# Kernel optimization log

Hardware: AMD Instinct MI355X
Metric: run time of the kernel (lower is better)

Reference implementation:

```python
import jax, jax.numpy as jnp
import numpy as np

C = 64
C8 = C // 8
N, H, W = 4, 512, 512


def conv1x1(x, w, b):
    # x: [N,C,H,W], w: [O,C], b: [O]
    return jnp.einsum('nchw,oc->nohw', x, w) + b[None, :, None, None]


def time_attention(x, qw, qb, kw, kb, vw, vb, gamma):
    # attention over the H axis; feature dim is (C//8)*W
    q = conv1x1(x, qw, qb)                     # [N,C8,H,W]
    k = conv1x1(x, kw, kb)                     # [N,C8,H,W]
    v = conv1x1(x, vw, vb)                     # [N,C,H,W]
    energy = jnp.einsum('nchw,ncgw->nhg', q, k)   # [N,H,H]
    attn = jax.nn.softmax(energy, axis=-1)
    out = jnp.einsum('ncgw,nhg->nchw', v, attn)   # [N,C,H,W]
    return gamma * out + x


def freq_attention(x, qw, qb, kw, kb, vw, vb, gamma):
    # attention over the W axis; feature dim is (C//8)*H
    q = conv1x1(x, qw, qb)
    k = conv1x1(x, kw, kb)
    v = conv1x1(x, vw, vb)
    energy = jnp.einsum('nchw,nchv->nwv', q, k)   # [N,W,W]
    attn = jax.nn.softmax(energy, axis=-1)
    out = jnp.einsum('nchv,nwv->nchw', v, attn)
    return gamma * out + x


def setup_inputs() -> dict:
    key = jax.random.key(0)
    ks = jax.random.split(key, 8)
    s = 0.05
    return {
        'x': jax.random.normal(ks[0], (N, C, H, W), dtype=jnp.float32),
        'tq_w': jax.random.normal(ks[1], (C8, C), dtype=jnp.float32) * s,
        'tq_b': jnp.zeros((C8,), jnp.float32),
        'tk_w': jax.random.normal(ks[2], (C8, C), dtype=jnp.float32) * s,
        'tk_b': jnp.zeros((C8,), jnp.float32),
        'tv_w': jax.random.normal(ks[3], (C, C), dtype=jnp.float32) * s,
        'tv_b': jnp.zeros((C,), jnp.float32),
        't_gamma': jnp.ones((1,), jnp.float32) * 0.5,
        'fq_w': jax.random.normal(ks[4], (C8, C), dtype=jnp.float32) * s,
        'fq_b': jnp.zeros((C8,), jnp.float32),
        'fk_w': jax.random.normal(ks[5], (C8, C), dtype=jnp.float32) * s,
        'fk_b': jnp.zeros((C8,), jnp.float32),
        'fv_w': jax.random.normal(ks[6], (C, C), dtype=jnp.float32) * s,
        'fv_b': jnp.zeros((C,), jnp.float32),
        'f_gamma': jnp.ones((1,), jnp.float32) * 0.5,
    }


def reference(x, tq_w, tq_b, tk_w, tk_b, tv_w, tv_b, t_gamma,
              fq_w, fq_b, fk_w, fk_b, fv_w, fv_b, f_gamma):
    t = time_attention(x, tq_w, tq_b, tk_w, tk_b, tv_w, tv_b, t_gamma)
    f = freq_attention(x, fq_w, fq_b, fk_w, fk_b, fv_w, fv_b, f_gamma)
    return x + t + f
```

## Files before the change

kernel.cpp:

```cpp
#include <hip/hip_runtime.h>
#include <stdint.h>

#define HW 262144
#define LDIM 512

typedef __bf16 bf16x8 __attribute__((ext_vector_type(8)));
typedef float f32x4 __attribute__((ext_vector_type(4)));
typedef short s16x8 __attribute__((ext_vector_type(8)));
typedef short s16x4 __attribute__((ext_vector_type(4)));

__device__ __forceinline__ unsigned short f2bf(float f) {
  union { float f; unsigned u; } v; v.f = f;
  unsigned r = v.u + 0x7fffu + ((v.u >> 16) & 1u);
  return (unsigned short)(r >> 16);
}

__device__ __forceinline__ float bf2f(short s) {
  union { unsigned u; float f; } v;
  v.u = ((unsigned)(unsigned short)s) << 16;
  return v.f;
}

__device__ __forceinline__ s16x8 pack_bf8(float4 a, float4 b) {
  s16x8 r;
  r[0] = (short)f2bf(a.x); r[1] = (short)f2bf(a.y);
  r[2] = (short)f2bf(a.z); r[3] = (short)f2bf(a.w);
  r[4] = (short)f2bf(b.x); r[5] = (short)f2bf(b.y);
  r[6] = (short)f2bf(b.z); r[7] = (short)f2bf(b.w);
  return r;
}

__device__ __forceinline__ f32x4 mfma16(bf16x8 a, bf16x8 b, f32x4 c) {
  return __builtin_amdgcn_mfma_f32_16x16x32_bf16(a, b, c, 0, 0, 0);
}

__device__ __forceinline__ void gl_lds16(const short* g, short* l) {
  __builtin_amdgcn_global_load_lds(
      (const __attribute__((address_space(1))) void*)g,
      (__attribute__((address_space(3))) void*)l, 16, 0, 0);
}

__global__ __launch_bounds__(256) void cast_k(const float* __restrict__ x,
                                              short* __restrict__ xb,
                                              short* __restrict__ xt) {
  __shared__ short L[64][72];
  int z = blockIdx.z;
  int h0 = blockIdx.y * 64, w0 = blockIdx.x * 64;
  int tid = threadIdx.x;
  size_t base = (size_t)z * HW;
  int hl = tid >> 4;
  int wl = (tid & 15) * 4;
#pragma unroll
  for (int it = 0; it < 4; ++it) {
    int h = h0 + hl + it * 16;
    float4 v = *(const float4*)(x + base + (size_t)h * 512 + w0 + wl);
    s16x4 b;
    b[0] = (short)f2bf(v.x); b[1] = (short)f2bf(v.y);
    b[2] = (short)f2bf(v.z); b[3] = (short)f2bf(v.w);
    *(s16x4*)(xb + base + (size_t)h * 512 + w0 + wl) = b;
    L[wl + 0][hl + it * 16] = b[0];
    L[wl + 1][hl + it * 16] = b[1];
    L[wl + 2][hl + it * 16] = b[2];
    L[wl + 3][hl + it * 16] = b[3];
  }
  __syncthreads();
#pragma unroll
  for (int it = 0; it < 4; ++it) {
    int w = hl + it * 16;
    s16x4 v = *(const s16x4*)(&L[w][wl]);
    *(s16x4*)(xt + base + (size_t)(w0 + w) * 512 + h0 + wl) = v;
  }
}

__global__ __launch_bounds__(256) void prep_k(const float* __restrict__ tvw,
                                              const float* __restrict__ fvw,
                                              short* __restrict__ Wvb) {
  int t = threadIdx.x;
#pragma unroll
  for (int i = 0; i < 2; ++i) {
    int idx = (i * 256 + t) * 8;
    float4 a = *(const float4*)(tvw + idx);
    float4 b = *(const float4*)(tvw + idx + 4);
    *(s16x8*)(Wvb + idx) = pack_bf8(a, b);
    a = *(const float4*)(fvw + idx);
    b = *(const float4*)(fvw + idx + 4);
    *(s16x8*)(Wvb + 4096 + idx) = pack_bf8(a, b);
  }
}

template<bool OBF>
__global__ __launch_bounds__(256, 4) void gemm_a(
    const short* __restrict__ A0, long az, int zshA,
    const short* __restrict__ B0, long bz, int zshB,
    void* __restrict__ C0, long cz) {
  __shared__ __align__(16) short As[128 * 32];
  __shared__ __align__(16) short Bs[128 * 32];
  int tid = threadIdx.x;
  int z = blockIdx.z;
  int m0g = blockIdx.y * 128, n0g = blockIdx.x * 128;
  const short* Abz = A0 + (size_t)(z >> zshA) * (size_t)az;
  const short* Bbz = B0 + (size_t)(z >> zshB) * (size_t)bz;
  int lane = tid & 63, wv = tid >> 6;
  int wm = (wv >> 1) * 64, wn = (wv & 1) * 64;
  int fr = lane & 15, q = lane >> 4;

  int srow = lane >> 2;
  int sch = (lane & 3) * 8;
  const short* ga0 = Abz + (size_t)(m0g + wv * 32 + srow) * 512 + sch;
  const short* ga1 = ga0 + 16 * 512;
  const short* gb0 = Bbz + (size_t)(n0g + wv * 32 + srow) * 512 + sch;
  const short* gb1 = gb0 + 16 * 512;
  short* la0 = As + (wv * 32) * 32;
  short* la1 = As + (wv * 32 + 16) * 32;
  short* lb0 = Bs + (wv * 32) * 32;
  short* lb1 = Bs + (wv * 32 + 16) * 32;

  f32x4 acc[4][4];
#pragma unroll
  for (int mi = 0; mi < 4; ++mi)
#pragma unroll
    for (int ni = 0; ni < 4; ++ni) acc[mi][ni] = (f32x4){0.f, 0.f, 0.f, 0.f};

  for (int kk = 0; kk < 512; kk += 32) {
    gl_lds16(ga0 + kk, la0);
    gl_lds16(ga1 + kk, la1);
    gl_lds16(gb0 + kk, lb0);
    gl_lds16(gb1 + kk, lb1);
    __syncthreads();
    bf16x8 af[4], bg[4];
#pragma unroll
    for (int mi = 0; mi < 4; ++mi)
      af[mi] = *(const bf16x8*)(As + (wm + mi * 16 + fr) * 32 + q * 8);
#pragma unroll
    for (int ni = 0; ni < 4; ++ni)
      bg[ni] = *(const bf16x8*)(Bs + (wn + ni * 16 + fr) * 32 + q * 8);
#pragma unroll
    for (int mi = 0; mi < 4; ++mi)
#pragma unroll
      for (int ni = 0; ni < 4; ++ni)
        acc[mi][ni] = mfma16(af[mi], bg[ni], acc[mi][ni]);
    __syncthreads();
  }

  size_t coff = (size_t)z * (size_t)cz;
#pragma unroll
  for (int mi = 0; mi < 4; ++mi)
#pragma unroll
    for (int ni = 0; ni < 4; ++ni) {
      int row = m0g + wm + mi * 16 + q * 4;
      int col = n0g + wn + ni * 16 + fr;
#pragma unroll
      for (int r = 0; r < 4; ++r) {
        float v = acc[mi][ni][r];
        if constexpr (OBF) {
          ((short*)C0)[coff + (size_t)(row + r) * LDIM + col] = (short)f2bf(v);
        } else {
          ((float*)C0)[coff + (size_t)(row + r) * LDIM + col] = v;
        }
      }
    }
}

__global__ __launch_bounds__(256, 2) void gemm_t(
    const short* __restrict__ A0, long az,
    const short* __restrict__ B0, long bz,
    float* __restrict__ C0, long cz) {
  __shared__ __align__(16) short As[128 * 40];
  __shared__ __align__(16) short Bs[128 * 40];
  int tid = threadIdx.x;
  int z = blockIdx.z;
  int m0g = blockIdx.y * 128, n0g = blockIdx.x * 128;
  const short* Abz = A0 + (size_t)z * (size_t)az;
  const short* Bbz = B0 + (size_t)z * (size_t)bz;
  int lane = tid & 63, wv = tid >> 6;
  int wm = (wv >> 1) * 64, wn = (wv & 1) * 64;
  int fr = lane & 15, q = lane >> 4;
  int mp = (tid & 63) * 2, k0 = (tid >> 6) * 8;

  f32x4 acc[4][4];
#pragma unroll
  for (int mi = 0; mi < 4; ++mi)
#pragma unroll
    for (int ni = 0; ni < 4; ++ni) acc[mi][ni] = (f32x4){0.f, 0.f, 0.f, 0.f};

  for (int kk = 0; kk < 512; kk += 32) {
    {
      const short* s = Abz + (size_t)(kk + k0) * 512 + m0g + mp;
      s16x8 c0, c1;
#pragma unroll
      for (int j = 0; j < 8; ++j) {
        unsigned v = *(const unsigned*)(s + (size_t)j * 512);
        c0[j] = (short)(v & 0xffffu);
        c1[j] = (short)(v >> 16);
      }
      *(s16x8*)(As + mp * 40 + k0) = c0;
      *(s16x8*)(As + (mp + 1) * 40 + k0) = c1;
    }
    {
      const short* s = Bbz + (size_t)(kk + k0) * 512 + n0g + mp;
      s16x8 c0, c1;
#pragma unroll
      for (int j = 0; j < 8; ++j) {
        unsigned v = *(const unsigned*)(s + (size_t)j * 512);
        c0[j] = (short)(v & 0xffffu);
        c1[j] = (short)(v >> 16);
      }
      *(s16x8*)(Bs + mp * 40 + k0) = c0;
      *(s16x8*)(Bs + (mp + 1) * 40 + k0) = c1;
    }
    __syncthreads();
    bf16x8 af[4], bg[4];
#pragma unroll
    for (int mi = 0; mi < 4; ++mi)
      af[mi] = *(const bf16x8*)(As + (wm + mi * 16 + fr) * 40 + q * 8);
#pragma unroll
    for (int ni = 0; ni < 4; ++ni)
      bg[ni] = *(const bf16x8*)(Bs + (wn + ni * 16 + fr) * 40 + q * 8);
#pragma unroll
    for (int mi = 0; mi < 4; ++mi)
#pragma unroll
      for (int ni = 0; ni < 4; ++ni)
        acc[mi][ni] = mfma16(af[mi], bg[ni], acc[mi][ni]);
    __syncthreads();
  }

  size_t coff = (size_t)z * (size_t)cz;
#pragma unroll
  for (int mi = 0; mi < 4; ++mi)
#pragma unroll
    for (int ni = 0; ni < 4; ++ni) {
      int row = m0g + wm + mi * 16 + q * 4;
      int col = n0g + wn + ni * 16 + fr;
#pragma unroll
      for (int r = 0; r < 4; ++r)
        C0[coff + (size_t)(row + r) * LDIM + col] = acc[mi][ni][r];
    }
}

__global__ __launch_bounds__(256, 2) void conv_qk_k(
    const short* __restrict__ xb,
    const float* __restrict__ tqw, const float* __restrict__ tqb,
    const float* __restrict__ tkw, const float* __restrict__ tkb,
    const float* __restrict__ fqw, const float* __restrict__ fqb,
    const float* __restrict__ fkw, const float* __restrict__ fkb,
    short* __restrict__ QT, short* __restrict__ KT,
    short* __restrict__ QF, short* __restrict__ KF) {
  __shared__ __align__(16) short As[128 * 72];
  __shared__ __align__(16) short Ws[32 * 72];
  __shared__ float bia[32];
  int tid = threadIdx.x;
  int n = blockIdx.x >> 11;
  int p0 = (blockIdx.x & 2047) << 7;
  {
    int co = tid >> 3, k0 = (tid & 7) * 8;
    const float* wsrc = (co < 8) ? tqw : (co < 16) ? tkw : (co < 24) ? fqw : fkw;
    const float* sp = wsrc + (co & 7) * 64 + k0;
    float4 f0 = *(const float4*)sp;
    float4 f1 = *(const float4*)(sp + 4);
    *(s16x8*)(Ws + co * 72 + k0) = pack_bf8(f0, f1);
    if (tid < 32) {
      const float* bsrc = (tid < 8) ? tqb : (tid < 16) ? tkb : (tid < 24) ? fqb : fkb;
      bia[tid] = bsrc[tid & 7];
    }
  }
  {
    int mp = (tid & 31) * 4, k0 = (tid >> 5) * 8;
    const short* sp = xb + ((size_t)(n * 64 + k0)) * HW + p0 + mp;
    s16x8 t0, t1, t2, t3;
#pragma unroll
    for (int j = 0; j < 8; ++j) {
      s16x4 vv = *(const s16x4*)(sp + (size_t)j * HW);
      t0[j] = vv[0]; t1[j] = vv[1]; t2[j] = vv[2]; t3[j] = vv[3];
    }
    *(s16x8*)(As + (mp + 0) * 72 + k0) = t0;
    *(s16x8*)(As + (mp + 1) * 72 + k0) = t1;
    *(s16x8*)(As + (mp + 2) * 72 + k0) = t2;
    *(s16x8*)(As + (mp + 3) * 72 + k0) = t3;
  }
  __syncthreads();
  int lane = tid & 63, wv = tid >> 6, fr = lane & 15, q = lane >> 4;
  int wm = wv * 32;
  f32x4 acc[2][2];
#pragma unroll
  for (int mi = 0; mi < 2; ++mi)
#pragma unroll
    for (int ni = 0; ni < 2; ++ni) acc[mi][ni] = (f32x4){0.f, 0.f, 0.f, 0.f};
#pragma unroll
  for (int ks = 0; ks < 2; ++ks) {
    bf16x8 af[2], bf_[2];
#pragma unroll
    for (int mi = 0; mi < 2; ++mi)
      af[mi] = *(const bf16x8*)(As + (wm + mi * 16 + fr) * 72 + ks * 32 + q * 8);
#pragma unroll
    for (int ni = 0; ni < 2; ++ni)
      bf_[ni] = *(const bf16x8*)(Ws + (ni * 16 + fr) * 72 + ks * 32 + q * 8);
#pragma unroll
    for (int mi = 0; mi < 2; ++mi)
#pragma unroll
      for (int ni = 0; ni < 2; ++ni)
        acc[mi][ni] = mfma16(af[mi], bf_[ni], acc[mi][ni]);
  }
#pragma unroll
  for (int mi = 0; mi < 2; ++mi)
#pragma unroll
    for (int ni = 0; ni < 2; ++ni) {
      int pl = wm + mi * 16 + q * 4;
      int co = ni * 16 + fr;
      float b = bia[co];
      short* dstt = (co < 8) ? QT : (co < 16) ? KT : (co < 24) ? QF : KF;
      short* d = dstt + ((size_t)(n * 8 + (co & 7))) * HW + p0 + pl;
      s16x4 sv;
#pragma unroll
      for (int r = 0; r < 4; ++r) sv[r] = (short)f2bf(acc[mi][ni][r] + b);
      *(s16x4*)d = sv;
    }
}

__global__ __launch_bounds__(256, 4) void softmax8_k(const float* __restrict__ Ep,
                                                     short* __restrict__ A) {
  int tid = threadIdx.x;
  int lane = tid & 63, wv = tid >> 6;
  int row = blockIdx.x * 4 + wv;
  int n = row >> 9, h = row & 511;
  const float* base = Ep + (size_t)(n * 8) * HW + (size_t)h * 512 + lane * 8;
  float v[8] = {0.f, 0.f, 0.f, 0.f, 0.f, 0.f, 0.f, 0.f};
#pragma unroll
  for (int cc = 0; cc < 8; ++cc) {
    const float* e = base + (size_t)cc * HW;
    float4 a = *(const float4*)e;
    float4 b = *(const float4*)(e + 4);
    v[0] += a.x; v[1] += a.y; v[2] += a.z; v[3] += a.w;
    v[4] += b.x; v[5] += b.y; v[6] += b.z; v[7] += b.w;
  }
  float m = v[0];
#pragma unroll
  for (int j = 1; j < 8; ++j) m = fmaxf(m, v[j]);
#pragma unroll
  for (int off = 32; off >= 1; off >>= 1) m = fmaxf(m, __shfl_xor(m, off));
  float s = 0.f;
#pragma unroll
  for (int j = 0; j < 8; ++j) {
    v[j] = __expf(v[j] - m);
    s += v[j];
  }
#pragma unroll
  for (int off = 32; off >= 1; off >>= 1) s += __shfl_xor(s, off);
  float inv = 1.f / s;
  s16x8 o;
#pragma unroll
  for (int j = 0; j < 8; ++j) o[j] = (short)f2bf(v[j] * inv);
  *(s16x8*)(A + (size_t)row * LDIM + lane * 8) = o;
}

__global__ __launch_bounds__(256, 3) void final_k(
    const short* __restrict__ ZT, const short* __restrict__ ZF,
    const short* __restrict__ xb, const short* __restrict__ Wvb,
    const float* __restrict__ tvb, const float* __restrict__ fvb,
    const float* __restrict__ tg, const float* __restrict__ fg,
    float* __restrict__ outn) {
  __shared__ __align__(16) short Zts[128 * 72];
  __shared__ __align__(16) short Zfs[128 * 72];
  __shared__ float bia[128];
  int tid = threadIdx.x;
  int n = blockIdx.x >> 11;
  int p0 = (blockIdx.x & 2047) << 7;
  if (tid < 128) bia[tid] = (tid < 64) ? tvb[tid] : fvb[tid - 64];
  {
    int mp = (tid & 31) * 4, k0 = (tid >> 5) * 8;
    const short* spT = ZT + ((size_t)(n * 64 + k0)) * HW + p0 + mp;
    const short* spF = ZF + ((size_t)(n * 64 + k0)) * HW + p0 + mp;
    s16x8 t0, t1, t2, t3;
#pragma unroll
    for (int j = 0; j < 8; ++j) {
      s16x4 vv = *(const s16x4*)(spT + (size_t)j * HW);
      t0[j] = vv[0]; t1[j] = vv[1]; t2[j] = vv[2]; t3[j] = vv[3];
    }
    *(s16x8*)(Zts + (mp + 0) * 72 + k0) = t0;
    *(s16x8*)(Zts + (mp + 1) * 72 + k0) = t1;
    *(s16x8*)(Zts + (mp + 2) * 72 + k0) = t2;
    *(s16x8*)(Zts + (mp + 3) * 72 + k0) = t3;
#pragma unroll
    for (int j = 0; j < 8; ++j) {
      s16x4 vv = *(const s16x4*)(spF + (size_t)j * HW);
      t0[j] = vv[0]; t1[j] = vv[1]; t2[j] = vv[2]; t3[j] = vv[3];
    }
    *(s16x8*)(Zfs + (mp + 0) * 72 + k0) = t0;
    *(s16x8*)(Zfs + (mp + 1) * 72 + k0) = t1;
    *(s16x8*)(Zfs + (mp + 2) * 72 + k0) = t2;
    *(s16x8*)(Zfs + (mp + 3) * 72 + k0) = t3;
  }
  __syncthreads();
  int lane = tid & 63, wv = tid >> 6, fr = lane & 15, q = lane >> 4;
  int wm = wv * 32;
  f32x4 at_[2][4], af_[2][4];
#pragma unroll
  for (int mi = 0; mi < 2; ++mi)
#pragma unroll
    for (int ni = 0; ni < 4; ++ni) {
      at_[mi][ni] = (f32x4){0.f, 0.f, 0.f, 0.f};
      af_[mi][ni] = (f32x4){0.f, 0.f, 0.f, 0.f};
    }
#pragma unroll
  for (int ks = 0; ks < 2; ++ks) {
    bf16x8 zt_[2], zf_[2], wt_[4], wf_[4];
#pragma unroll
    for (int mi = 0; mi < 2; ++mi) {
      zt_[mi] = *(const bf16x8*)(Zts + (wm + mi * 16 + fr) * 72 + ks * 32 + q * 8);
      zf_[mi] = *(const bf16x8*)(Zfs + (wm + mi * 16 + fr) * 72 + ks * 32 + q * 8);
    }
#pragma unroll
    for (int ni = 0; ni < 4; ++ni) {
      wt_[ni] = *(const bf16x8*)(Wvb + (ni * 16 + fr) * 64 + ks * 32 + q * 8);
      wf_[ni] = *(const bf16x8*)(Wvb + 4096 + (ni * 16 + fr) * 64 + ks * 32 + q * 8);
    }
#pragma unroll
    for (int mi = 0; mi < 2; ++mi)
#pragma unroll
      for (int ni = 0; ni < 4; ++ni) {
        at_[mi][ni] = mfma16(zt_[mi], wt_[ni], at_[mi][ni]);
        af_[mi][ni] = mfma16(zf_[mi], wf_[ni], af_[mi][ni]);
      }
  }
  float gtv = tg[0], gfv = fg[0];
#pragma unroll
  for (int mi = 0; mi < 2; ++mi)
#pragma unroll
    for (int ni = 0; ni < 4; ++ni) {
      int pl = wm + mi * 16 + q * 4;
      int co = ni * 16 + fr;
      size_t idx = ((size_t)(n * 64 + co)) * HW + p0 + pl;
      s16x4 xv = *(const s16x4*)(xb + idx);
      float bt = bia[co], bff = bia[64 + co];
      float4 ov;
      ov.x = 3.f * bf2f(xv[0]) + gtv * (at_[mi][ni][0] + bt) + gfv * (af_[mi][ni][0] + bff);
      ov.y = 3.f * bf2f(xv[1]) + gtv * (at_[mi][ni][1] + bt) + gfv * (af_[mi][ni][1] + bff);
      ov.z = 3.f * bf2f(xv[2]) + gtv * (at_[mi][ni][2] + bt) + gfv * (af_[mi][ni][2] + bff);
      ov.w = 3.f * bf2f(xv[3]) + gtv * (at_[mi][ni][3] + bt) + gfv * (af_[mi][ni][3] + bff);
      *(float4*)(outn + idx) = ov;
    }
}

extern "C" void kernel_launch(void* const* d_in, const int* in_sizes, int n_in,
                              void* d_out, int out_size, void* d_ws, size_t ws_size,
                              hipStream_t stream) {
  (void)in_sizes; (void)n_in; (void)out_size;
  const float* x   = (const float*)d_in[0];
  const float* tqw = (const float*)d_in[1];
  const float* tqb = (const float*)d_in[2];
  const float* tkw = (const float*)d_in[3];
  const float* tkb = (const float*)d_in[4];
  const float* tvw = (const float*)d_in[5];
  const float* tvb = (const float*)d_in[6];
  const float* tg  = (const float*)d_in[7];
  const float* fqw = (const float*)d_in[8];
  const float* fqb = (const float*)d_in[9];
  const float* fkw = (const float*)d_in[10];
  const float* fkb = (const float*)d_in[11];
  const float* fvw = (const float*)d_in[12];
  const float* fvb = (const float*)d_in[13];
  const float* fg  = (const float*)d_in[14];
  float* out = (float*)d_out;

  const size_t per_n = ((size_t)64 * HW * 2) * 3
                     + ((size_t)8 * HW * 2) * 4
                     + (size_t)HW * 2;
  int nb = (ws_size >= 4 * per_n + 16384) ? 4
         : (ws_size >= 2 * per_n + 16384) ? 2 : 1;

  char* w = (char*)d_ws;
  short* Wvb = (short*)w;
  char* wb = w + 16384;
  size_t sz_x  = (size_t)nb * 64 * HW * 2;
  size_t sz_qk = (size_t)nb * 8 * HW * 2;
  short* xb = (short*)(wb);
  short* ZF = (short*)(wb + sz_x);
  short* xt = ZF;
  short* QT = (short*)(wb + 2 * sz_x);
  short* KT = (short*)(wb + 2 * sz_x + sz_qk);
  short* QF = (short*)(wb + 2 * sz_x + 2 * sz_qk);
  short* KF = (short*)(wb + 2 * sz_x + 3 * sz_qk);
  short* ZT = (short*)(wb + 2 * sz_x + 4 * sz_qk);
  short* Ab = (short*)(wb + 3 * sz_x + 4 * sz_qk);
  float* EbT = (float*)ZT;
  float* EbF = (float*)ZF;

  prep_k<<<dim3(1), dim3(256), 0, stream>>>(tvw, fvw, Wvb);

  for (int n0 = 0; n0 < 4; n0 += nb) {
    const float* xn = x + (size_t)n0 * 64 * HW;
    float* outn = out + (size_t)n0 * 64 * HW;
    cast_k<<<dim3(8, 8, nb * 64), dim3(256), 0, stream>>>(xn, xb, xt);
    conv_qk_k<<<dim3(nb * 2048), dim3(256), 0, stream>>>(
        xb, tqw, tqb, tkw, tkb, fqw, fqb, fkw, fkb, QT, KT, QF, KF);
    gemm_a<false><<<dim3(4, 4, nb * 8), dim3(256), 0, stream>>>(
        QT, (long)HW, 0, KT, (long)HW, 0, EbT, (long)HW);
    softmax8_k<<<dim3(nb * 128), dim3(256), 0, stream>>>(EbT, Ab);
    gemm_a<true><<<dim3(4, 4, nb * 64), dim3(256), 0, stream>>>(
        Ab, (long)HW, 6, xt, (long)HW, 0, ZT, (long)HW);
    gemm_t<<<dim3(4, 4, nb * 8), dim3(256), 0, stream>>>(
        QF, (long)HW, KF, (long)HW, EbF, (long)HW);
    softmax8_k<<<dim3(nb * 128), dim3(256), 0, stream>>>(EbF, Ab);
    gemm_a<true><<<dim3(4, 4, nb * 64), dim3(256), 0, stream>>>(
        xb, (long)HW, 0, Ab, (long)HW, 6, ZF, (long)HW);
    final_k<<<dim3(nb * 2048), dim3(256), 0, stream>>>(
        ZT, ZF, xb, Wvb, tvb, fvb, tg, fg, outn);
  }
}
```

Baseline: 977.1 us.

## Apply value projections before attention and fuse both attention GEMMs with output epilogue

Reorders the computation so the 1x1 value convolutions run before the attention products: frequency V is computed alongside Q/K in one conv kernel, and time V is computed in place on the transposed input. The two attention GEMMs then accumulate into one register tile in a single fused kernel that also adds the residual and biases and writes the fp32 output, which removes the separate final projection kernel and the ZT/ZF intermediates. Gamma is folded into the softmax normalisation, and the energy scratch buffers are placed in the output tensor. The cost is an extra V-conv pass over the input, a loop that stages four tiles per k-step and so uses more LDS, and scalar strided epilogue stores in place of vectorised ones.

```diff
diff --git a/kernel.cpp b/kernel.cpp
--- a/kernel.cpp
+++ b/kernel.cpp
@@ -72,20 +72,163 @@
   }
 }
 
-__global__ __launch_bounds__(256) void prep_k(const float* __restrict__ tvw,
-                                              const float* __restrict__ fvw,
-                                              short* __restrict__ Wvb) {
-  int t = threadIdx.x;
+__global__ __launch_bounds__(256, 2) void conv_qkvf_k(
+    const short* __restrict__ xb,
+    const float* __restrict__ tqw, const float* __restrict__ tqb,
+    const float* __restrict__ tkw, const float* __restrict__ tkb,
+    const float* __restrict__ fqw, const float* __restrict__ fqb,
+    const float* __restrict__ fkw, const float* __restrict__ fkb,
+    const float* __restrict__ fvw,
+    short* __restrict__ QT, short* __restrict__ KT,
+    short* __restrict__ QF, short* __restrict__ KF,
+    short* __restrict__ Vf) {
+  __shared__ __align__(16) short As[128 * 72];
+  __shared__ __align__(16) short Ws[96 * 72];
+  __shared__ float bia[32];
+  int tid = threadIdx.x;
+  int n = blockIdx.x >> 11;
+  int p0 = (blockIdx.x & 2047) << 7;
+#pragma unroll
+  for (int i = 0; i < 3; ++i) {
+    int idx = i * 256 + tid;
+    int co = idx >> 3, k0 = (idx & 7) * 8;
+    const float* wrow = (co < 8)  ? tqw + co * 64
+                      : (co < 16) ? tkw + (co - 8) * 64
+                      : (co < 24) ? fqw + (co - 16) * 64
+                      : (co < 32) ? fkw + (co - 24) * 64
+                                  : fvw + (co - 32) * 64;
+    float4 f0 = *(const float4*)(wrow + k0);
+    float4 f1 = *(const float4*)(wrow + k0 + 4);
+    *(s16x8*)(Ws + co * 72 + k0) = pack_bf8(f0, f1);
+  }
+  if (tid < 32) {
+    const float* bsrc = (tid < 8) ? tqb : (tid < 16) ? tkb : (tid < 24) ? fqb : fkb;
+    bia[tid] = bsrc[tid & 7];
+  }
+  {
+    int mp = (tid & 31) * 4, k0 = (tid >> 5) * 8;
+    const short* sp = xb + ((size_t)(n * 64 + k0)) * HW + p0 + mp;
+    s16x8 t0, t1, t2, t3;
+#pragma unroll
+    for (int j = 0; j < 8; ++j) {
+      s16x4 vv = *(const s16x4*)(sp + (size_t)j * HW);
+      t0[j] = vv[0]; t1[j] = vv[1]; t2[j] = vv[2]; t3[j] = vv[3];
+    }
+    *(s16x8*)(As + (mp + 0) * 72 + k0) = t0;
+    *(s16x8*)(As + (mp + 1) * 72 + k0) = t1;
+    *(s16x8*)(As + (mp + 2) * 72 + k0) = t2;
+    *(s16x8*)(As + (mp + 3) * 72 + k0) = t3;
+  }
+  __syncthreads();
+  int lane = tid & 63, wv = tid >> 6, fr = lane & 15, q = lane >> 4;
+  int wm = wv * 32;
+  f32x4 acc[2][6];
+#pragma unroll
+  for (int mi = 0; mi < 2; ++mi)
+#pragma unroll
+    for (int ni = 0; ni < 6; ++ni) acc[mi][ni] = (f32x4){0.f, 0.f, 0.f, 0.f};
+#pragma unroll
+  for (int ks = 0; ks < 2; ++ks) {
+    bf16x8 af[2], bw[6];
+#pragma unroll
+    for (int mi = 0; mi < 2; ++mi)
+      af[mi] = *(const bf16x8*)(As + (wm + mi * 16 + fr) * 72 + ks * 32 + q * 8);
+#pragma unroll
+    for (int ni = 0; ni < 6; ++ni)
+      bw[ni] = *(const bf16x8*)(Ws + (ni * 16 + fr) * 72 + ks * 32 + q * 8);
+#pragma unroll
+    for (int mi = 0; mi < 2; ++mi)
+#pragma unroll
+      for (int ni = 0; ni < 6; ++ni)
+        acc[mi][ni] = mfma16(af[mi], bw[ni], acc[mi][ni]);
+  }
+#pragma unroll
+  for (int mi = 0; mi < 2; ++mi)
+#pragma unroll
+    for (int ni = 0; ni < 6; ++ni) {
+      int pl = wm + mi * 16 + q * 4;
+      int co = ni * 16 + fr;
+      float b = 0.f;
+      short* dst;
+      if (co < 32) {
+        b = bia[co];
+        short* dd = (co < 8) ? QT : (co < 16) ? KT : (co < 24) ? QF : KF;
+        dst = dd + ((size_t)(n * 8 + (co & 7))) * HW;
+      } else {
+        dst = Vf + ((size_t)(n * 64 + (co - 32))) * HW;
+      }
+      s16x4 sv;
+#pragma unroll
+      for (int r = 0; r < 4; ++r) sv[r] = (short)f2bf(acc[mi][ni][r] + b);
+      *(s16x4*)(dst + p0 + pl) = sv;
+    }
+}
+
+__global__ __launch_bounds__(256, 2) void conv_v_k(
+    const short* xin, const float* __restrict__ w64, short* vout) {
+  __shared__ __align__(16) short As[128 * 72];
+  __shared__ __align__(16) short Ws[64 * 72];
+  int tid = threadIdx.x;
+  int n = blockIdx.x >> 11;
+  int p0 = (blockIdx.x & 2047) << 7;
 #pragma unroll
   for (int i = 0; i < 2; ++i) {
-    int idx = (i * 256 + t) * 8;
-    float4 a = *(const float4*)(tvw + idx);
-    float4 b = *(const float4*)(tvw + idx + 4);
-    *(s16x8*)(Wvb + idx) = pack_bf8(a, b);
-    a = *(const float4*)(fvw + idx);
-    b = *(const float4*)(fvw + idx + 4);
-    *(s16x8*)(Wvb + 4096 + idx) = pack_bf8(a, b);
-  }
+    int idx = i * 256 + tid;
+    int co = idx >> 3, k0 = (idx & 7) * 8;
+    const float* wrow = w64 + co * 64;
+    float4 f0 = *(const float4*)(wrow + k0);
+    float4 f1 = *(const float4*)(wrow + k0 + 4);
+    *(s16x8*)(Ws + co * 72 + k0) = pack_bf8(f0, f1);
+  }
+  {
+    int mp = (tid & 31) * 4, k0 = (tid >> 5) * 8;
+    const short* sp = xin + ((size_t)(n * 64 + k0)) * HW + p0 + mp;
+    s16x8 t0, t1, t2, t3;
+#pragma unroll
+    for (int j = 0; j < 8; ++j) {
+      s16x4 vv = *(const s16x4*)(sp + (size_t)j * HW);
+      t0[j] = vv[0]; t1[j] = vv[1]; t2[j] = vv[2]; t3[j] = vv[3];
+    }
+    *(s16x8*)(As + (mp + 0) * 72 + k0) = t0;
+    *(s16x8*)(As + (mp + 1) * 72 + k0) = t1;
+    *(s16x8*)(As + (mp + 2) * 72 + k0) = t2;
+    *(s16x8*)(As + (mp + 3) * 72 + k0) = t3;
+  }
+  __syncthreads();
+  int lane = tid & 63, wv = tid >> 6, fr = lane & 15, q = lane >> 4;
+  int wm = wv * 32;
+  f32x4 acc[2][4];
+#pragma unroll
+  for (int mi = 0; mi < 2; ++mi)
+#pragma unroll
+    for (int ni = 0; ni < 4; ++ni) acc[mi][ni] = (f32x4){0.f, 0.f, 0.f, 0.f};
+#pragma unroll
+  for (int ks = 0; ks < 2; ++ks) {
+    bf16x8 af[2], bw[4];
+#pragma unroll
+    for (int mi = 0; mi < 2; ++mi)
+      af[mi] = *(const bf16x8*)(As + (wm + mi * 16 + fr) * 72 + ks * 32 + q * 8);
+#pragma unroll
+    for (int ni = 0; ni < 4; ++ni)
+      bw[ni] = *(const bf16x8*)(Ws + (ni * 16 + fr) * 72 + ks * 32 + q * 8);
+#pragma unroll
+    for (int mi = 0; mi < 2; ++mi)
+#pragma unroll
+      for (int ni = 0; ni < 4; ++ni)
+        acc[mi][ni] = mfma16(af[mi], bw[ni], acc[mi][ni]);
+  }
+#pragma unroll
+  for (int mi = 0; mi < 2; ++mi)
+#pragma unroll
+    for (int ni = 0; ni < 4; ++ni) {
+      int pl = wm + mi * 16 + q * 4;
+      int co = ni * 16 + fr;
+      short* d = vout + ((size_t)(n * 64 + co)) * HW + p0 + pl;
+      s16x4 sv;
+#pragma unroll
+      for (int r = 0; r < 4; ++r) sv[r] = (short)f2bf(acc[mi][ni][r]);
+      *(s16x4*)d = sv;
+    }
 }
 
 template<bool OBF>
@@ -237,86 +380,8 @@
     }
 }
 
-__global__ __launch_bounds__(256, 2) void conv_qk_k(
-    const short* __restrict__ xb,
-    const float* __restrict__ tqw, const float* __restrict__ tqb,
-    const float* __restrict__ tkw, const float* __restrict__ tkb,
-    const float* __restrict__ fqw, const float* __restrict__ fqb,
-    const float* __restrict__ fkw, const float* __restrict__ fkb,
-    short* __restrict__ QT, short* __restrict__ KT,
-    short* __restrict__ QF, short* __restrict__ KF) {
-  __shared__ __align__(16) short As[128 * 72];
-  __shared__ __align__(16) short Ws[32 * 72];
-  __shared__ float bia[32];
-  int tid = threadIdx.x;
-  int n = blockIdx.x >> 11;
-  int p0 = (blockIdx.x & 2047) << 7;
-  {
-    int co = tid >> 3, k0 = (tid & 7) * 8;
-    const float* wsrc = (co < 8) ? tqw : (co < 16) ? tkw : (co < 24) ? fqw : fkw;
-    const float* sp = wsrc + (co & 7) * 64 + k0;
-    float4 f0 = *(const float4*)sp;
-    float4 f1 = *(const float4*)(sp + 4);
-    *(s16x8*)(Ws + co * 72 + k0) = pack_bf8(f0, f1);
-    if (tid < 32) {
-      const float* bsrc = (tid < 8) ? tqb : (tid < 16) ? tkb : (tid < 24) ? fqb : fkb;
-      bia[tid] = bsrc[tid & 7];
-    }
-  }
-  {
-    int mp = (tid & 31) * 4, k0 = (tid >> 5) * 8;
-    const short* sp = xb + ((size_t)(n * 64 + k0)) * HW + p0 + mp;
-    s16x8 t0, t1, t2, t3;
-#pragma unroll
-    for (int j = 0; j < 8; ++j) {
-      s16x4 vv = *(const s16x4*)(sp + (size_t)j * HW);
-      t0[j] = vv[0]; t1[j] = vv[1]; t2[j] = vv[2]; t3[j] = vv[3];
-    }
-    *(s16x8*)(As + (mp + 0) * 72 + k0) = t0;
-    *(s16x8*)(As + (mp + 1) * 72 + k0) = t1;
-    *(s16x8*)(As + (mp + 2) * 72 + k0) = t2;
-    *(s16x8*)(As + (mp + 3) * 72 + k0) = t3;
-  }
-  __syncthreads();
-  int lane = tid & 63, wv = tid >> 6, fr = lane & 15, q = lane >> 4;
-  int wm = wv * 32;
-  f32x4 acc[2][2];
-#pragma unroll
-  for (int mi = 0; mi < 2; ++mi)
-#pragma unroll
-    for (int ni = 0; ni < 2; ++ni) acc[mi][ni] = (f32x4){0.f, 0.f, 0.f, 0.f};
-#pragma unroll
-  for (int ks = 0; ks < 2; ++ks) {
-    bf16x8 af[2], bf_[2];
-#pragma unroll
-    for (int mi = 0; mi < 2; ++mi)
-      af[mi] = *(const bf16x8*)(As + (wm + mi * 16 + fr) * 72 + ks * 32 + q * 8);
-#pragma unroll
-    for (int ni = 0; ni < 2; ++ni)
-      bf_[ni] = *(const bf16x8*)(Ws + (ni * 16 + fr) * 72 + ks * 32 + q * 8);
-#pragma unroll
-    for (int mi = 0; mi < 2; ++mi)
-#pragma unroll
-      for (int ni = 0; ni < 2; ++ni)
-        acc[mi][ni] = mfma16(af[mi], bf_[ni], acc[mi][ni]);
-  }
-#pragma unroll
-  for (int mi = 0; mi < 2; ++mi)
-#pragma unroll
-    for (int ni = 0; ni < 2; ++ni) {
-      int pl = wm + mi * 16 + q * 4;
-      int co = ni * 16 + fr;
-      float b = bia[co];
-      short* dstt = (co < 8) ? QT : (co < 16) ? KT : (co < 24) ? QF : KF;
-      short* d = dstt + ((size_t)(n * 8 + (co & 7))) * HW + p0 + pl;
-      s16x4 sv;
-#pragma unroll
-      for (int r = 0; r < 4; ++r) sv[r] = (short)f2bf(acc[mi][ni][r] + b);
-      *(s16x4*)d = sv;
-    }
-}
-
 __global__ __launch_bounds__(256, 4) void softmax8_k(const float* __restrict__ Ep,
+                                                     const float* __restrict__ gp,
                                                      short* __restrict__ A) {
   int tid = threadIdx.x;
   int lane = tid & 63, wv = tid >> 6;
@@ -345,98 +410,107 @@
   }
 #pragma unroll
   for (int off = 32; off >= 1; off >>= 1) s += __shfl_xor(s, off);
-  float inv = 1.f / s;
+  float sc = gp[0] / s;
   s16x8 o;
 #pragma unroll
-  for (int j = 0; j < 8; ++j) o[j] = (short)f2bf(v[j] * inv);
+  for (int j = 0; j < 8; ++j) o[j] = (short)f2bf(v[j] * sc);
   *(s16x8*)(A + (size_t)row * LDIM + lane * 8) = o;
 }
 
-__global__ __launch_bounds__(256, 3) void final_k(
-    const short* __restrict__ ZT, const short* __restrict__ ZF,
-    const short* __restrict__ xb, const short* __restrict__ Wvb,
+__global__ __launch_bounds__(256, 3) void gemm_tf(
+    const short* __restrict__ At, const short* __restrict__ Vt,
+    const short* __restrict__ Vf, const short* __restrict__ Af,
+    const short* __restrict__ xb,
     const float* __restrict__ tvb, const float* __restrict__ fvb,
     const float* __restrict__ tg, const float* __restrict__ fg,
-    float* __restrict__ outn) {
-  __shared__ __align__(16) short Zts[128 * 72];
-  __shared__ __align__(16) short Zfs[128 * 72];
-  __shared__ float bia[128];
-  int tid = threadIdx.x;
-  int n = blockIdx.x >> 11;
-  int p0 = (blockIdx.x & 2047) << 7;
-  if (tid < 128) bia[tid] = (tid < 64) ? tvb[tid] : fvb[tid - 64];
-  {
-    int mp = (tid & 31) * 4, k0 = (tid >> 5) * 8;
-    const short* spT = ZT + ((size_t)(n * 64 + k0)) * HW + p0 + mp;
-    const short* spF = ZF + ((size_t)(n * 64 + k0)) * HW + p0 + mp;
-    s16x8 t0, t1, t2, t3;
-#pragma unroll
-    for (int j = 0; j < 8; ++j) {
-      s16x4 vv = *(const s16x4*)(spT + (size_t)j * HW);
-      t0[j] = vv[0]; t1[j] = vv[1]; t2[j] = vv[2]; t3[j] = vv[3];
-    }
-    *(s16x8*)(Zts + (mp + 0) * 72 + k0) = t0;
-    *(s16x8*)(Zts + (mp + 1) * 72 + k0) = t1;
-    *(s16x8*)(Zts + (mp + 2) * 72 + k0) = t2;
-    *(s16x8*)(Zts + (mp + 3) * 72 + k0) = t3;
-#pragma unroll
-    for (int j = 0; j < 8; ++j) {
-      s16x4 vv = *(const s16x4*)(spF + (size_t)j * HW);
-      t0[j] = vv[0]; t1[j] = vv[1]; t2[j] = vv[2]; t3[j] = vv[3];
-    }
-    *(s16x8*)(Zfs + (mp + 0) * 72 + k0) = t0;
-    *(s16x8*)(Zfs + (mp + 1) * 72 + k0) = t1;
-    *(s16x8*)(Zfs + (mp + 2) * 72 + k0) = t2;
-    *(s16x8*)(Zfs + (mp + 3) * 72 + k0) = t3;
-  }
-  __syncthreads();
-  int lane = tid & 63, wv = tid >> 6, fr = lane & 15, q = lane >> 4;
-  int wm = wv * 32;
-  f32x4 at_[2][4], af_[2][4];
-#pragma unroll
-  for (int mi = 0; mi < 2; ++mi)
+    float* __restrict__ out) {
+  __shared__ __align__(16) short As1[128 * 32];
+  __shared__ __align__(16) short Bs1[128 * 32];
+  __shared__ __align__(16) short As2[128 * 32];
+  __shared__ __align__(16) short Bs2[128 * 32];
+  int tid = threadIdx.x;
+  int z = blockIdx.z;
+  int n = z >> 6, o = z & 63;
+  int m0g = blockIdx.y * 128, n0g = blockIdx.x * 128;
+  const short* A1 = At + (size_t)n * HW;
+  const short* B1 = Vt + (size_t)z * HW;
+  const short* A2 = Vf + (size_t)z * HW;
+  const short* B2 = Af + (size_t)n * HW;
+  int lane = tid & 63, wv = tid >> 6;
+  int wm = (wv >> 1) * 64, wn = (wv & 1) * 64;
+  int fr = lane & 15, q = lane >> 4;
+
+  int srow = lane >> 2;
+  int sch = (lane & 3) * 8;
+  const short* g1a = A1 + (size_t)(m0g + wv * 32 + srow) * 512 + sch;
+  const short* g1b = B1 + (size_t)(n0g + wv * 32 + srow) * 512 + sch;
+  const short* g2a = A2 + (size_t)(m0g + wv * 32 + srow) * 512 + sch;
+  const short* g2b = B2 + (size_t)(n0g + wv * 32 + srow) * 512 + sch;
+  short* l1a = As1 + (wv * 32) * 32;
+  short* l1b = Bs1 + (wv * 32) * 32;
+  short* l2a = As2 + (wv * 32) * 32;
+  short* l2b = Bs2 + (wv * 32) * 32;
+
+  f32x4 acc[4][4];
+#pragma unroll
+  for (int mi = 0; mi < 4; ++mi)
+#pragma unroll
+    for (int ni = 0; ni < 4; ++ni) acc[mi][ni] = (f32x4){0.f, 0.f, 0.f, 0.f};
+
+  for (int kk = 0; kk < 512; kk += 32) {
+    gl_lds16(g1a + kk, l1a);
+    gl_lds16(g1a + kk + 16 * 512, l1a + 16 * 32);
+    gl_lds16(g1b + kk, l1b);
+    gl_lds16(g1b + kk + 16 * 512, l1b + 16 * 32);
+    gl_lds16(g2a + kk, l2a);
+    gl_lds16(g2a + kk + 16 * 512, l2a + 16 * 32);
+    gl_lds16(g2b + kk, l2b);
+    gl_lds16(g2b + kk + 16 * 512, l2b + 16 * 32);
+    __syncthreads();
+    {
+      bf16x8 a1[4], b1[4];
+#pragma unroll
+      for (int mi = 0; mi < 4; ++mi)
+        a1[mi] = *(const bf16x8*)(As1 + (wm + mi * 16 + fr) * 32 + q * 8);
+#pragma unroll
+      for (int ni = 0; ni < 4; ++ni)
+        b1[ni] = *(const bf16x8*)(Bs1 + (wn + ni * 16 + fr) * 32 + q * 8);
+#pragma unroll
+      for (int mi = 0; mi < 4; ++mi)
+#pragma unroll
+        for (int ni = 0; ni < 4; ++ni)
+          acc[mi][ni] = mfma16(a1[mi], b1[ni], acc[mi][ni]);
+    }
+    {
+      bf16x8 a2[4], b2[4];
+#pragma unroll
+      for (int mi = 0; mi < 4; ++mi)
+        a2[mi] = *(const bf16x8*)(As2 + (wm + mi * 16 + fr) * 32 + q * 8);
+#pragma unroll
+      for (int ni = 0; ni < 4; ++ni)
+        b2[ni] = *(const bf16x8*)(Bs2 + (wn + ni * 16 + fr) * 32 + q * 8);
+#pragma unroll
+      for (int mi = 0; mi < 4; ++mi)
+#pragma unroll
+        for (int ni = 0; ni < 4; ++ni)
+          acc[mi][ni] = mfma16(a2[mi], b2[ni], acc[mi][ni]);
+    }
+    __syncthreads();
+  }
+
+  float cb = tg[0] * tvb[o] + fg[0] * fvb[o];
+  size_t zoff = (size_t)z * HW;
+#pragma unroll
+  for (int mi = 0; mi < 4; ++mi)
 #pragma unroll
     for (int ni = 0; ni < 4; ++ni) {
-      at_[mi][ni] = (f32x4){0.f, 0.f, 0.f, 0.f};
-      af_[mi][ni] = (f32x4){0.f, 0.f, 0.f, 0.f};
-    }
-#pragma unroll
-  for (int ks = 0; ks < 2; ++ks) {
-    bf16x8 zt_[2], zf_[2], wt_[4], wf_[4];
-#pragma unroll
-    for (int mi = 0; mi < 2; ++mi) {
-      zt_[mi] = *(const bf16x8*)(Zts + (wm + mi * 16 + fr) * 72 + ks * 32 + q * 8);
-      zf_[mi] = *(const bf16x8*)(Zfs + (wm + mi * 16 + fr) * 72 + ks * 32 + q * 8);
-    }
-#pragma unroll
-    for (int ni = 0; ni < 4; ++ni) {
-      wt_[ni] = *(const bf16x8*)(Wvb + (ni * 16 + fr) * 64 + ks * 32 + q * 8);
-      wf_[ni] = *(const bf16x8*)(Wvb + 4096 + (ni * 16 + fr) * 64 + ks * 32 + q * 8);
-    }
-#pragma unroll
-    for (int mi = 0; mi < 2; ++mi)
-#pragma unroll
-      for (int ni = 0; ni < 4; ++ni) {
-        at_[mi][ni] = mfma16(zt_[mi], wt_[ni], at_[mi][ni]);
-        af_[mi][ni] = mfma16(zf_[mi], wf_[ni], af_[mi][ni]);
+      int row = m0g + wm + mi * 16 + q * 4;
+      int col = n0g + wn + ni * 16 + fr;
+#pragma unroll
+      for (int r = 0; r < 4; ++r) {
+        size_t idx = zoff + (size_t)(row + r) * LDIM + col;
+        out[idx] = 3.f * bf2f(xb[idx]) + acc[mi][ni][r] + cb;
       }
-  }
-  float gtv = tg[0], gfv = fg[0];
-#pragma unroll
-  for (int mi = 0; mi < 2; ++mi)
-#pragma unroll
-    for (int ni = 0; ni < 4; ++ni) {
-      int pl = wm + mi * 16 + q * 4;
-      int co = ni * 16 + fr;
-      size_t idx = ((size_t)(n * 64 + co)) * HW + p0 + pl;
-      s16x4 xv = *(const s16x4*)(xb + idx);
-      float bt = bia[co], bff = bia[64 + co];
-      float4 ov;
-      ov.x = 3.f * bf2f(xv[0]) + gtv * (at_[mi][ni][0] + bt) + gfv * (af_[mi][ni][0] + bff);
-      ov.y = 3.f * bf2f(xv[1]) + gtv * (at_[mi][ni][1] + bt) + gfv * (af_[mi][ni][1] + bff);
-      ov.z = 3.f * bf2f(xv[2]) + gtv * (at_[mi][ni][2] + bt) + gfv * (af_[mi][ni][2] + bff);
-      ov.w = 3.f * bf2f(xv[3]) + gtv * (at_[mi][ni][3] + bt) + gfv * (af_[mi][ni][3] + bff);
-      *(float4*)(outn + idx) = ov;
     }
 }
 
@@ -462,47 +536,40 @@
   float* out = (float*)d_out;
 
   const size_t per_n = ((size_t)64 * HW * 2) * 3
-                     + ((size_t)8 * HW * 2) * 4
-                     + (size_t)HW * 2;
-  int nb = (ws_size >= 4 * per_n + 16384) ? 4
-         : (ws_size >= 2 * per_n + 16384) ? 2 : 1;
-
-  char* w = (char*)d_ws;
-  short* Wvb = (short*)w;
-  char* wb = w + 16384;
+                     + ((size_t)8 * HW * 2) * 4;
+  int nb = (ws_size >= 4 * per_n) ? 4
+         : (ws_size >= 2 * per_n) ? 2 : 1;
+
+  char* wb = (char*)d_ws;
   size_t sz_x  = (size_t)nb * 64 * HW * 2;
   size_t sz_qk = (size_t)nb * 8 * HW * 2;
   short* xb = (short*)(wb);
-  short* ZF = (short*)(wb + sz_x);
-  short* xt = ZF;
-  short* QT = (short*)(wb + 2 * sz_x);
-  short* KT = (short*)(wb + 2 * sz_x + sz_qk);
-  short* QF = (short*)(wb + 2 * sz_x + 2 * sz_qk);
-  short* KF = (short*)(wb + 2 * sz_x + 3 * sz_qk);
-  short* ZT = (short*)(wb + 2 * sz_x + 4 * sz_qk);
-  short* Ab = (short*)(wb + 3 * sz_x + 4 * sz_qk);
-  float* EbT = (float*)ZT;
-  float* EbF = (float*)ZF;
-
-  prep_k<<<dim3(1), dim3(256), 0, stream>>>(tvw, fvw, Wvb);
+  short* xt = (short*)(wb + sz_x);
+  short* Vf = (short*)(wb + 2 * sz_x);
+  short* QT = (short*)(wb + 3 * sz_x);
+  short* KT = (short*)(wb + 3 * sz_x + sz_qk);
+  short* QF = (short*)(wb + 3 * sz_x + 2 * sz_qk);
+  short* KF = (short*)(wb + 3 * sz_x + 3 * sz_qk);
+  short* At = QT;
+  short* Af = QF;
 
   for (int n0 = 0; n0 < 4; n0 += nb) {
     const float* xn = x + (size_t)n0 * 64 * HW;
     float* outn = out + (size_t)n0 * 64 * HW;
+    float* EbT = outn;
+    float* EbF = outn + (size_t)nb * 8 * HW;
+
     cast_k<<<dim3(8, 8, nb * 64), dim3(256), 0, stream>>>(xn, xb, xt);
-    conv_qk_k<<<dim3(nb * 2048), dim3(256), 0, stream>>>(
-        xb, tqw, tqb, tkw, tkb, fqw, fqb, fkw, fkb, QT, KT, QF, KF);
+    conv_qkvf_k<<<dim3(nb * 2048), dim3(256), 0, stream>>>(
+        xb, tqw, tqb, tkw, tkb, fqw, fqb, fkw, fkb, fvw, QT, KT, QF, KF, Vf);
+    conv_v_k<<<dim3(nb * 2048), dim3(256), 0, stream>>>(xt, tvw, xt);
     gemm_a<false><<<dim3(4, 4, nb * 8), dim3(256), 0, stream>>>(
         QT, (long)HW, 0, KT, (long)HW, 0, EbT, (long)HW);
-    softmax8_k<<<dim3(nb * 128), dim3(256), 0, stream>>>(EbT, Ab);
-    gemm_a<true><<<dim3(4, 4, nb * 64), dim3(256), 0, stream>>>(
-        Ab, (long)HW, 6, xt, (long)HW, 0, ZT, (long)HW);
+    softmax8_k<<<dim3(nb * 128), dim3(256), 0, stream>>>(EbT, tg, At);
     gemm_t<<<dim3(4, 4, nb * 8), dim3(256), 0, stream>>>(
         QF, (long)HW, KF, (long)HW, EbF, (long)HW);
-    softmax8_k<<<dim3(nb * 128), dim3(256), 0, stream>>>(EbF, Ab);
-    gemm_a<true><<<dim3(4, 4, nb * 64), dim3(256), 0, stream>>>(
-        xb, (long)HW, 0, Ab, (long)HW, 6, ZF, (long)HW);
-    final_k<<<dim3(nb * 2048), dim3(256), 0, stream>>>(
-        ZT, ZF, xb, Wvb, tvb, fvb, tg, fg, outn);
-  }
-}
+    softmax8_k<<<dim3(nb * 128), dim3(256), 0, stream>>>(EbF, fg, Af);
+    gemm_tf<<<dim3(4, 4, nb * 64), dim3(256), 0, stream>>>(
+        At, xt, Vf, Af, xb, tvb, fvb, tg, fg, outn);
+  }
+}
```

New measurement: 954.4 us. -2.3%, faster.
